# Performance work log

Hardware: AMD Instinct MI355X
Metric: run time of the kernel (lower is better)

The kernel has to match this reference:

```python
import jax, jax.numpy as jnp
import numpy as np

DIST_IND = 7.0        # disturbance_indicator
SLOPE_MIN, SLOPE_MAX = 0.0, 2.0
MAX_INTERCEPT = 100.0  # max_intercept / max_intercept_after_disturbance


def setup_inputs() -> dict:
    key = jax.random.key(0)
    k1, k2 = jax.random.split(key)
    # canopy-height-like values so year-over-year diffs < -7 occur (disturbances)
    out = jax.random.normal(k1, (8, 2, 30, 256, 256), dtype=jnp.float32) * 20.0 + 40.0
    target = jax.random.normal(k2, (8, 30, 256, 256), dtype=jnp.float32)
    return {"out": out, "target": target}


def _fit_segment(y, mask, x, n):
    """Masked OLS fit per pixel. y, mask, x: (B,Y,H,W); x is the local time index
    (pre-masked). n: (B,H,W) segment length. Returns fitted (B,Y,H,W), slope (B,H,W)."""
    n_safe = jnp.maximum(n, 1.0)
    mean_x = (x * mask).sum(1) / n_safe            # (B,H,W)
    mean_y = (y * mask).sum(1) / n_safe
    cov = ((x - mean_x[:, None]) * (y - mean_y[:, None]) * mask).sum(1)
    var = n * (n * n - 1.0) / 12.0                 # sum (x-mean_x)^2 for x=0..n-1
    slope = jnp.where(var > 0, cov / jnp.maximum(var, 1.0), 0.0)
    intercept = jnp.clip(mean_y - slope * mean_x, 0.0, MAX_INTERCEPT)
    fitted = jnp.clip(slope, SLOPE_MIN, SLOPE_MAX)[:, None] * x + intercept[:, None]
    return fitted, slope


def _forward(out, target):
    out0 = jax.lax.stop_gradient(out[:, 0])
    out1 = out[:, 1]
    B, Y, H, W = out0.shape
    # disturbance index: argmin over [-7, diff_1, ..., diff_{Y-1}] with entries 1, Y-1 zeroed
    diff = jnp.diff(out0, axis=1)
    diff = jnp.concatenate([jnp.full((B, 1, H, W), -DIST_IND, out0.dtype), diff], axis=1)
    diff = diff.at[:, 1].set(0.0).at[:, -1].set(0.0)  # full_disturbance_window=False
    d = jnp.argmin(diff, axis=1)                       # (B,H,W), first-min like torch
    t = jnp.arange(Y, dtype=out0.dtype)[None, :, None, None]
    df = d[:, None].astype(out0.dtype)                 # (B,1,H,W)
    mask_b = (t < df).astype(out0.dtype)               # before-disturbance timesteps
    mask_a = 1.0 - mask_b                              # from disturbance onward
    n_b = df[:, 0]
    n_a = Y - n_b
    fitted_b, _ = _fit_segment(out0, mask_b, t * mask_b, n_b)
    fitted_a, _ = _fit_segment(out0, mask_a, (t - df) * mask_a, n_a)
    fitted = jnp.where(mask_b > 0, fitted_b, fitted_a)  # piecewise fit, detached
    # use_l2=True; disturbance_factor == no_disturbance_factor == 1 -> plain mean
    loss = ((fitted - out1) ** 2).mean(axis=1).mean()
    return loss


def reference(out, target):
    return _forward(out, target)
```

## Files before the change

kernel.cpp:

```cpp
#include <hip/hip_runtime.h>

#define YDIM 30
#define PLANE4 16384
#define NTHR 256
#define NBLK 512

__global__ __launch_bounds__(NTHR) void drl_main(const float4* __restrict__ out,
                                                 float* __restrict__ partial) {
    const int g = blockIdx.x * NTHR + threadIdx.x;
    const int b = g >> 14;
    const int hw4 = g & 16383;

    const float4* p0 = out + (size_t)b * (2 * YDIM * PLANE4) + hw4;
    const float4* p1 = p0 + YDIM * PLANE4;

    float run_s [4] = {0.f,0.f,0.f,0.f};
    float run_sx[4] = {0.f,0.f,0.f,0.f};
    float snap_s [4] = {0.f,0.f,0.f,0.f};
    float snap_sx[4] = {0.f,0.f,0.f,0.f};
    float best[4] = {-7.f,-7.f,-7.f,-7.f};
    float fd  [4] = {0.f,0.f,0.f,0.f};
    float prev[4];

#pragma unroll
    for (int y = 0; y < YDIM; ++y) {
        float4 v = p0[y * PLANE4];
        float cur[4] = {v.x, v.y, v.z, v.w};
        if (y >= 2 && y <= YDIM - 2) {
#pragma unroll
            for (int c = 0; c < 4; ++c) {
                float df = cur[c] - prev[c];
                bool lt = df < best[c];
                best[c]    = lt ? df         : best[c];
                fd[c]      = lt ? (float)y   : fd[c];
                snap_s[c]  = lt ? run_s[c]   : snap_s[c];
                snap_sx[c] = lt ? run_sx[c]  : snap_sx[c];
            }
        }
#pragma unroll
        for (int c = 0; c < 4; ++c) {
            run_s[c]  += cur[c];
            run_sx[c]  = fmaf((float)y, cur[c], run_sx[c]);
            prev[c]    = cur[c];
        }
    }

    float sc_b[4], itc_b[4], sc_a[4], itc_a[4];
#pragma unroll
    for (int c = 0; c < 4; ++c) {
        float nb  = fd[c];
        float na  = (float)YDIM - nb;
        float nsb = fmaxf(nb, 1.f);
        float sy_b  = snap_s[c];
        float sxy_b = snap_sx[c];
        float sy_a  = run_s[c]  - sy_b;
        float sxy_a = (run_sx[c] - snap_sx[c]) - nb * sy_a;
        float mxb = nb * (nb - 1.f) * 0.5f / nsb;
        float myb = sy_b / nsb;
        float mxa = na * (na - 1.f) * 0.5f / na;
        float mya = sy_a / na;
        float cov_b = sxy_b - mxb * sy_b;
        float cov_a = sxy_a - mxa * sy_a;
        float var_b = nb * (nb * nb - 1.f) * (1.f / 12.f);
        float var_a = na * (na * na - 1.f) * (1.f / 12.f);
        float slope_b = (var_b > 0.f) ? cov_b / fmaxf(var_b, 1.f) : 0.f;
        float slope_a = (var_a > 0.f) ? cov_a / fmaxf(var_a, 1.f) : 0.f;
        itc_b[c] = fminf(fmaxf(myb - slope_b * mxb, 0.f), 100.f);
        itc_a[c] = fminf(fmaxf(mya - slope_a * mxa, 0.f), 100.f);
        sc_b[c]  = fminf(fmaxf(slope_b, 0.f), 2.f);
        sc_a[c]  = fminf(fmaxf(slope_a, 0.f), 2.f);
    }

    float acc[4] = {0.f,0.f,0.f,0.f};
#pragma unroll
    for (int y = 0; y < YDIM; ++y) {
        float4 v = p1[y * PLANE4];
        float t1[4] = {v.x, v.y, v.z, v.w};
#pragma unroll
        for (int c = 0; c < 4; ++c) {
            float xf  = (float)y;
            float fb  = fmaf(sc_b[c], xf,          itc_b[c]);
            float fa  = fmaf(sc_a[c], xf - fd[c],  itc_a[c]);
            float fit = (xf < fd[c]) ? fb : fa;
            float e   = fit - t1[c];
            acc[c]    = fmaf(e, e, acc[c]);
        }
    }
    float a = (acc[0] + acc[1]) + (acc[2] + acc[3]);

#pragma unroll
    for (int off = 32; off > 0; off >>= 1) a += __shfl_down(a, off, 64);
    __shared__ float wsum[NTHR / 64];
    if ((threadIdx.x & 63) == 0) wsum[threadIdx.x >> 6] = a;
    __syncthreads();
    if (threadIdx.x == 0)
        partial[blockIdx.x] = (wsum[0] + wsum[1]) + (wsum[2] + wsum[3]);
}

__global__ __launch_bounds__(NTHR) void drl_reduce(const float* __restrict__ partial,
                                                   float* __restrict__ outp) {
    double s = 0.0;
    for (int i = threadIdx.x; i < NBLK; i += NTHR) s += (double)partial[i];
    __shared__ double sm[NTHR];
    sm[threadIdx.x] = s;
    __syncthreads();
    for (int st = NTHR / 2; st > 0; st >>= 1) {
        if (threadIdx.x < st) sm[threadIdx.x] += sm[threadIdx.x + st];
        __syncthreads();
    }
    if (threadIdx.x == 0) {
        const double N = (double)(8 * YDIM) * 65536.0;
        outp[0] = (float)(sm[0] / N);
    }
}

extern "C" void kernel_launch(void* const* d_in, const int* in_sizes, int n_in,
                              void* d_out, int out_size, void* d_ws, size_t ws_size,
                              hipStream_t stream) {
    const float4* out_t = (const float4*)d_in[0];
    float* partial = (float*)d_ws;
    float* loss    = (float*)d_out;

    drl_main<<<NBLK, NTHR, 0, stream>>>(out_t, partial);
    drl_reduce<<<1, NTHR, 0, stream>>>(partial, loss);
}
```

Baseline: 28.68 us.

## Expand squared error algebraically in one pass and fuse final reduction via last-block atomic

The squared-error loss is expanded into closed-form sums: target sums (S, Sx, Sxx) are accumulated together with the regression sums in a single pass that snapshots at the disturbance index. This removes the second time loop and lets both planes be loaded together, so more loads are in flight. The separate reduce kernel is replaced by an atomic counter and a last-block reduction, with a memset added to reset the counter. Expanding the squares risks float cancellation error, and the memset adds its own launch.

```diff
diff --git a/kernel.cpp b/kernel.cpp
--- a/kernel.cpp
+++ b/kernel.cpp
@@ -4,9 +4,12 @@
 #define PLANE4 16384
 #define NTHR 256
 #define NBLK 512
+#define NPIX 15728640.0
 
-__global__ __launch_bounds__(NTHR) void drl_main(const float4* __restrict__ out,
-                                                 float* __restrict__ partial) {
+__global__ __launch_bounds__(NTHR) void drl_fused(const float4* __restrict__ out,
+                                                  unsigned int* __restrict__ cnt,
+                                                  float* __restrict__ partial,
+                                                  float* __restrict__ lossp) {
     const int g = blockIdx.x * NTHR + threadIdx.x;
     const int b = g >> 14;
     const int hw4 = g & 16383;
@@ -14,103 +17,113 @@
     const float4* p0 = out + (size_t)b * (2 * YDIM * PLANE4) + hw4;
     const float4* p1 = p0 + YDIM * PLANE4;
 
-    float run_s [4] = {0.f,0.f,0.f,0.f};
-    float run_sx[4] = {0.f,0.f,0.f,0.f};
-    float snap_s [4] = {0.f,0.f,0.f,0.f};
-    float snap_sx[4] = {0.f,0.f,0.f,0.f};
-    float best[4] = {-7.f,-7.f,-7.f,-7.f};
-    float fd  [4] = {0.f,0.f,0.f,0.f};
+    float run_s[4]={0,0,0,0}, run_sx[4]={0,0,0,0};
+    float s1[4]={0,0,0,0}, s1x[4]={0,0,0,0}, s1q[4]={0,0,0,0};
+    float sn_s[4]={0,0,0,0}, sn_sx[4]={0,0,0,0};
+    float sn_s1[4]={0,0,0,0}, sn_s1x[4]={0,0,0,0};
+    float best[4]={-7,-7,-7,-7};
+    float fd[4]={0,0,0,0};
     float prev[4];
 
 #pragma unroll
     for (int y = 0; y < YDIM; ++y) {
-        float4 v = p0[y * PLANE4];
-        float cur[4] = {v.x, v.y, v.z, v.w};
+        float4 v0 = p0[y * PLANE4];
+        float4 v1 = p1[y * PLANE4];
+        float c0[4] = {v0.x, v0.y, v0.z, v0.w};
+        float t1[4] = {v1.x, v1.y, v1.z, v1.w};
         if (y >= 2 && y <= YDIM - 2) {
 #pragma unroll
             for (int c = 0; c < 4; ++c) {
-                float df = cur[c] - prev[c];
+                float df = c0[c] - prev[c];
                 bool lt = df < best[c];
-                best[c]    = lt ? df         : best[c];
-                fd[c]      = lt ? (float)y   : fd[c];
-                snap_s[c]  = lt ? run_s[c]   : snap_s[c];
-                snap_sx[c] = lt ? run_sx[c]  : snap_sx[c];
+                best[c]  = lt ? df        : best[c];
+                fd[c]    = lt ? (float)y  : fd[c];
+                sn_s[c]  = lt ? run_s[c]  : sn_s[c];
+                sn_sx[c] = lt ? run_sx[c] : sn_sx[c];
+                sn_s1[c] = lt ? s1[c]     : sn_s1[c];
+                sn_s1x[c]= lt ? s1x[c]    : sn_s1x[c];
             }
         }
 #pragma unroll
         for (int c = 0; c < 4; ++c) {
-            run_s[c]  += cur[c];
-            run_sx[c]  = fmaf((float)y, cur[c], run_sx[c]);
-            prev[c]    = cur[c];
+            run_s[c] += c0[c];
+            run_sx[c] = fmaf((float)y, c0[c], run_sx[c]);
+            s1[c]    += t1[c];
+            s1x[c]    = fmaf((float)y, t1[c], s1x[c]);
+            s1q[c]    = fmaf(t1[c], t1[c], s1q[c]);
+            prev[c]   = c0[c];
         }
     }
 
-    float sc_b[4], itc_b[4], sc_a[4], itc_a[4];
+    float accT = 0.f;
 #pragma unroll
     for (int c = 0; c < 4; ++c) {
-        float nb  = fd[c];
-        float na  = (float)YDIM - nb;
+        float d   = fd[c];
+        float nb  = d;
+        float na  = (float)YDIM - d;
         float nsb = fmaxf(nb, 1.f);
-        float sy_b  = snap_s[c];
-        float sxy_b = snap_sx[c];
-        float sy_a  = run_s[c]  - sy_b;
-        float sxy_a = (run_sx[c] - snap_sx[c]) - nb * sy_a;
+        float Syb  = sn_s[c];
+        float Sxyb = sn_sx[c];
+        float Sya  = run_s[c] - sn_s[c];
+        float Sxya = fmaf(-d, Sya, run_sx[c] - sn_sx[c]);
         float mxb = nb * (nb - 1.f) * 0.5f / nsb;
-        float myb = sy_b / nsb;
-        float mxa = na * (na - 1.f) * 0.5f / na;
-        float mya = sy_a / na;
-        float cov_b = sxy_b - mxb * sy_b;
-        float cov_a = sxy_a - mxa * sy_a;
-        float var_b = nb * (nb * nb - 1.f) * (1.f / 12.f);
-        float var_a = na * (na * na - 1.f) * (1.f / 12.f);
-        float slope_b = (var_b > 0.f) ? cov_b / fmaxf(var_b, 1.f) : 0.f;
-        float slope_a = (var_a > 0.f) ? cov_a / fmaxf(var_a, 1.f) : 0.f;
-        itc_b[c] = fminf(fmaxf(myb - slope_b * mxb, 0.f), 100.f);
-        itc_a[c] = fminf(fmaxf(mya - slope_a * mxa, 0.f), 100.f);
-        sc_b[c]  = fminf(fmaxf(slope_b, 0.f), 2.f);
-        sc_a[c]  = fminf(fmaxf(slope_a, 0.f), 2.f);
+        float myb = Syb / nsb;
+        float mxa = (na - 1.f) * 0.5f;
+        float mya = Sya / na;
+        float covb = fmaf(-mxb, Syb, Sxyb);
+        float cova = fmaf(-mxa, Sya, Sxya);
+        float varb = nb * (nb * nb - 1.f) * (1.f / 12.f);
+        float vara = na * (na * na - 1.f) * (1.f / 12.f);
+        float slb = (varb > 0.f) ? covb / fmaxf(varb, 1.f) : 0.f;
+        float sla = (vara > 0.f) ? cova / fmaxf(vara, 1.f) : 0.f;
+        float ib = fminf(fmaxf(myb - slb * mxb, 0.f), 100.f);
+        float ia = fminf(fmaxf(mya - sla * mxa, 0.f), 100.f);
+        float qb = fminf(fmaxf(slb, 0.f), 2.f);
+        float qa = fminf(fmaxf(sla, 0.f), 2.f);
+        float Sy_b  = nb * (nb - 1.f) * 0.5f;
+        float Syy_b = nb * (nb - 1.f) * (2.f * nb - 1.f) * (1.f / 6.f);
+        float Sx_a  = na * (na - 1.f) * 0.5f;
+        float Sxx_a = na * (na - 1.f) * (2.f * na - 1.f) * (1.f / 6.f);
+        float T1b  = sn_s1[c];
+        float T1yb = sn_s1x[c];
+        float T1a  = s1[c] - sn_s1[c];
+        float T1xa = fmaf(-d, T1a, s1x[c] - sn_s1x[c]);
+        float Lb = qb * qb * Syy_b + 2.f * qb * ib * Sy_b + nb * ib * ib
+                 - 2.f * fmaf(qb, T1yb, ib * T1b);
+        float La = qa * qa * Sxx_a + 2.f * qa * ia * Sx_a + na * ia * ia
+                 - 2.f * fmaf(qa, T1xa, ia * T1a);
+        accT += Lb + La + s1q[c];
     }
 
-    float acc[4] = {0.f,0.f,0.f,0.f};
 #pragma unroll
-    for (int y = 0; y < YDIM; ++y) {
-        float4 v = p1[y * PLANE4];
-        float t1[4] = {v.x, v.y, v.z, v.w};
-#pragma unroll
-        for (int c = 0; c < 4; ++c) {
-            float xf  = (float)y;
-            float fb  = fmaf(sc_b[c], xf,          itc_b[c]);
-            float fa  = fmaf(sc_a[c], xf - fd[c],  itc_a[c]);
-            float fit = (xf < fd[c]) ? fb : fa;
-            float e   = fit - t1[c];
-            acc[c]    = fmaf(e, e, acc[c]);
+    for (int off = 32; off > 0; off >>= 1) accT += __shfl_down(accT, off, 64);
+    __shared__ float wsum[NTHR / 64];
+    __shared__ bool last;
+    if ((threadIdx.x & 63) == 0) wsum[threadIdx.x >> 6] = accT;
+    __syncthreads();
+    if (threadIdx.x == 0) {
+        float bs = (wsum[0] + wsum[1]) + (wsum[2] + wsum[3]);
+        __hip_atomic_store(&partial[blockIdx.x], bs, __ATOMIC_RELEASE,
+                           __HIP_MEMORY_SCOPE_AGENT);
+        unsigned int old = __hip_atomic_fetch_add(cnt, 1u, __ATOMIC_ACQ_REL,
+                                                  __HIP_MEMORY_SCOPE_AGENT);
+        last = (old == NBLK - 1);
+    }
+    __syncthreads();
+
+    if (last) {
+        double s = 0.0;
+        for (int i = threadIdx.x; i < NBLK; i += NTHR)
+            s += (double)__hip_atomic_load(&partial[i], __ATOMIC_ACQUIRE,
+                                           __HIP_MEMORY_SCOPE_AGENT);
+        __shared__ double sm[NTHR];
+        sm[threadIdx.x] = s;
+        __syncthreads();
+        for (int st = NTHR / 2; st > 0; st >>= 1) {
+            if (threadIdx.x < st) sm[threadIdx.x] += sm[threadIdx.x + st];
+            __syncthreads();
         }
-    }
-    float a = (acc[0] + acc[1]) + (acc[2] + acc[3]);
-
-#pragma unroll
-    for (int off = 32; off > 0; off >>= 1) a += __shfl_down(a, off, 64);
-    __shared__ float wsum[NTHR / 64];
-    if ((threadIdx.x & 63) == 0) wsum[threadIdx.x >> 6] = a;
-    __syncthreads();
-    if (threadIdx.x == 0)
-        partial[blockIdx.x] = (wsum[0] + wsum[1]) + (wsum[2] + wsum[3]);
-}
-
-__global__ __launch_bounds__(NTHR) void drl_reduce(const float* __restrict__ partial,
-                                                   float* __restrict__ outp) {
-    double s = 0.0;
-    for (int i = threadIdx.x; i < NBLK; i += NTHR) s += (double)partial[i];
-    __shared__ double sm[NTHR];
-    sm[threadIdx.x] = s;
-    __syncthreads();
-    for (int st = NTHR / 2; st > 0; st >>= 1) {
-        if (threadIdx.x < st) sm[threadIdx.x] += sm[threadIdx.x + st];
-        __syncthreads();
-    }
-    if (threadIdx.x == 0) {
-        const double N = (double)(8 * YDIM) * 65536.0;
-        outp[0] = (float)(sm[0] / N);
+        if (threadIdx.x == 0) lossp[0] = (float)(sm[0] / NPIX);
     }
 }
 
@@ -118,9 +131,10 @@
                               void* d_out, int out_size, void* d_ws, size_t ws_size,
                               hipStream_t stream) {
     const float4* out_t = (const float4*)d_in[0];
-    float* partial = (float*)d_ws;
+    unsigned int* cnt = (unsigned int*)d_ws;
+    float* partial = (float*)((char*)d_ws + 128);
     float* loss    = (float*)d_out;
 
-    drl_main<<<NBLK, NTHR, 0, stream>>>(out_t, partial);
-    drl_reduce<<<1, NTHR, 0, stream>>>(partial, loss);
+    hipMemsetAsync(d_ws, 0, 4, stream);
+    drl_fused<<<NBLK, NTHR, 0, stream>>>(out_t, cnt, partial, loss);
 }
```

After: 51.48 us. +79.5%, slower.
